# Optimization experiments

Measured on AMD Instinct MI355X. Metric: run time of the kernel, lower is better.

## Reference

```python
import jax, jax.numpy as jnp
import numpy as np

N_NODES = 100000
N_EDGES = 800000
NODE_DIM = 64
EDGE_DIM = 64
GEO_DIM = 8
GEO_OUT = 32
COND_DIM = 512
N_GRAPHS = 64
JOIN_DIM = EDGE_DIM + GEO_OUT  # 96


def setup_inputs() -> dict:
    key = jax.random.key(0)
    ks = jax.random.split(key, 10)
    return {
        "node_feats": jax.random.normal(ks[0], (N_NODES, NODE_DIM), jnp.float32),
        "edge_index": jax.random.randint(ks[1], (2, N_EDGES), 0, N_NODES, jnp.int64),
        "e_geo": jax.random.normal(ks[2], (N_EDGES, GEO_DIM), jnp.float32),
        "cond": jax.random.normal(ks[3], (N_GRAPHS, COND_DIM), jnp.float32),
        "edge_batch_ids": jax.random.randint(ks[4], (N_EDGES,), 0, N_GRAPHS, jnp.int64),
        "Wn": jax.random.normal(ks[5], (NODE_DIM, EDGE_DIM), jnp.float32) / np.sqrt(NODE_DIM),
        "bn": jnp.zeros((EDGE_DIM,), jnp.float32),
        "Wg": jax.random.normal(ks[6], (GEO_DIM, GEO_OUT), jnp.float32) / np.sqrt(GEO_DIM),
        "bg": jnp.zeros((GEO_OUT,), jnp.float32),
        "Wc": jax.random.normal(ks[7], (COND_DIM, 2 * EDGE_DIM), jnp.float32) / np.sqrt(COND_DIM),
        "bc": jnp.zeros((2 * EDGE_DIM,), jnp.float32),
        "Wx": jax.random.normal(ks[8], (JOIN_DIM, EDGE_DIM), jnp.float32) / np.sqrt(JOIN_DIM),
    }


def reference(node_feats, edge_index, e_geo, cond, edge_batch_ids,
              Wn, bn, Wg, bg, Wc, bc, Wx):
    # n_proj: project node features  [N, node_dim] -> [N, edge_dim]
    n_proj = node_feats @ Wn + bn
    # combine_node_attr 'mul': gather to edge endpoints and multiply  [E, edge_dim]
    src = n_proj[edge_index[0]]
    dst = n_proj[edge_index[1]]
    n_join = src * dst
    # e_geo_linear: [E, geo_dim] -> [E, geo_out]
    eg = e_geo @ Wg + bg
    # join features [E, edge_dim + geo_out]
    join = jnp.concatenate([n_join, eg], axis=-1)
    # FilmFusion: cond_proj -> gamma/beta per graph, gather to edges
    gb = cond @ Wc + bc                      # [B, 2*edge_dim]
    gamma, beta = jnp.split(gb, 2, axis=-1)
    gamma = gamma + 1.0
    gamma_e = gamma[edge_batch_ids]          # [E, edge_dim]
    beta_e = beta[edge_batch_ids]
    # x_linear (bias=False), FiLM modulation, relu
    x = join @ Wx
    return jax.nn.relu(x * gamma_e + beta_e)
```

## Files before the change

### kernel.cpp

```cpp
#include <hip/hip_runtime.h>

#define N_NODES   100000
#define N_EDGES   800000
#define NODE_DIM  64
#define EDGE_DIM  64
#define GEO_DIM   8
#define GEO_OUT   32
#define COND_DIM  512
#define N_GRAPHS  64

typedef short  bf8   __attribute__((ext_vector_type(8)));
typedef float  f32x4 __attribute__((ext_vector_type(4)));
typedef unsigned short u16x8 __attribute__((ext_vector_type(8)));

__device__ __forceinline__ float b2f(unsigned short u) {
    return __uint_as_float(((unsigned)u) << 16);
}
__device__ __forceinline__ short f2b(float f) {
    unsigned u = __float_as_uint(f);
    u = (u + 0x7FFFu + ((u >> 16) & 1u)) >> 16;
    return (short)u;
}
__device__ __forceinline__ float rdlane(float v, int l) {
    return __int_as_float(__builtin_amdgcn_readlane(__float_as_int(v), l));
}

__global__ __launch_bounds__(128) void prep_kernel(
        const float* __restrict__ cond, const float* __restrict__ Wc,
        const float* __restrict__ bc,   const float* __restrict__ Wg,
        const float* __restrict__ bg,   const float* __restrict__ Wx,
        float* __restrict__ gamma, float* __restrict__ beta2,
        unsigned short* __restrict__ Bmat) {
    int t = threadIdx.x;
    int g = blockIdx.x;
    if (g < N_GRAPHS) {
        __shared__ float condl[COND_DIM];
        __shared__ float gbl[128];
        for (int i = t; i < COND_DIM; i += 128) condl[i] = cond[g * COND_DIM + i];
        __syncthreads();
        float acc = bc[t];
        #pragma unroll 8
        for (int k = 0; k < COND_DIM; ++k) acc += condl[k] * Wc[k * 128 + t];
        gbl[t] = acc;
        __syncthreads();
        if (t < 64) {
            float gam = gbl[t] + 1.0f;
            float bet = gbl[64 + t];
            float cv = 0.0f;
            #pragma unroll
            for (int i = 0; i < GEO_OUT; ++i) cv += bg[i] * Wx[(64 + i) * 64 + t];
            gamma[g * 64 + t] = gam;
            beta2[g * 64 + t] = bet + cv * gam;
        }
    } else {
        for (int idx = t; idx < 64 * 64; idx += 128)
            Bmat[idx] = (unsigned short)f2b(Wx[idx]);
        for (int idx = t; idx < 8 * 64; idx += 128) {
            int r = idx >> 6, n = idx & 63;
            float s = 0.f;
            #pragma unroll
            for (int i = 0; i < GEO_OUT; ++i) s += Wg[r * GEO_OUT + i] * Wx[(64 + i) * 64 + n];
            Bmat[(64 + r) * 64 + n] = (unsigned short)f2b(s);
        }
        for (int idx = t; idx < 24 * 64; idx += 128)
            Bmat[72 * 64 + idx] = 0;
    }
}

__global__ __launch_bounds__(256) void nproj_kernel(
        const float* __restrict__ nf, const float* __restrict__ Wn,
        const float* __restrict__ bn, unsigned short* __restrict__ nprojb) {
    int lane = threadIdx.x & 63;
    int wid    = (blockIdx.x * blockDim.x + threadIdx.x) >> 6;
    int nwaves = (gridDim.x * blockDim.x) >> 6;
    float wcol[64];
    #pragma unroll
    for (int k = 0; k < 64; ++k) wcol[k] = Wn[k * 64 + lane];
    float bnl = bn[lane];
    for (int node = wid; node < N_NODES; node += nwaves) {
        float v = nf[(size_t)node * 64 + lane];
        float a0 = 0.f, a1 = 0.f, a2 = 0.f, a3 = bnl;
        #pragma unroll
        for (int k = 0; k < 64; k += 4) {
            a0 = fmaf(rdlane(v, k    ), wcol[k    ], a0);
            a1 = fmaf(rdlane(v, k + 1), wcol[k + 1], a1);
            a2 = fmaf(rdlane(v, k + 2), wcol[k + 2], a2);
            a3 = fmaf(rdlane(v, k + 3), wcol[k + 3], a3);
        }
        nprojb[(size_t)node * 64 + lane] = (unsigned short)f2b((a0 + a1) + (a2 + a3));
    }
}

__global__ __launch_bounds__(256) void edge_kernel(
        const unsigned short* __restrict__ nprojb,
        const int*   __restrict__ eidx,
        const float* __restrict__ egeo,
        const int*   __restrict__ ebatch,
        const unsigned short* __restrict__ Bmat,
        const float* __restrict__ gamma,
        const float* __restrict__ beta2,
        float* __restrict__ out) {
    int lane = threadIdx.x & 63;
    int q  = lane >> 4;
    int mm = lane & 15;
    int wid    = (blockIdx.x * blockDim.x + threadIdx.x) >> 6;
    int nwaves = (gridDim.x * blockDim.x) >> 6;

    bf8 bfrag[3][4];
    #pragma unroll
    for (int c = 0; c < 3; ++c)
        #pragma unroll
        for (int t = 0; t < 4; ++t)
            #pragma unroll
            for (int j = 0; j < 8; ++j)
                bfrag[c][t][j] = (short)Bmat[(c * 32 + q * 8 + j) * 64 + t * 16 + mm];

    const int NTILES = N_EDGES / 16;
    for (int tile = wid; tile < NTILES; tile += nwaves) {
        int e0 = tile * 16;
        int e  = e0 + mm;
        int s = __builtin_nontemporal_load(eidx + e);
        int d = __builtin_nontemporal_load(eidx + N_EDGES + e);
        const u16x8* ps = (const u16x8*)(nprojb + (size_t)s * 64 + q * 8);
        const u16x8* pd = (const u16x8*)(nprojb + (size_t)d * 64 + q * 8);
        u16x8 s0 = ps[0], s1 = ps[4];
        u16x8 d0 = pd[0], d1 = pd[4];
        bf8 a0, a1, a2;
        #pragma unroll
        for (int j = 0; j < 8; ++j) {
            a0[j] = f2b(b2f(s0[j]) * b2f(d0[j]));
            a1[j] = f2b(b2f(s1[j]) * b2f(d1[j]));
            a2[j] = 0;
        }
        if (q == 0) {
            f32x4 g0 = __builtin_nontemporal_load((const f32x4*)(egeo + (size_t)e * 8));
            f32x4 g1 = __builtin_nontemporal_load((const f32x4*)(egeo + (size_t)e * 8 + 4));
            #pragma unroll
            for (int j = 0; j < 4; ++j) { a2[j] = f2b(g0[j]); a2[4 + j] = f2b(g1[j]); }
        }

        f32x4 acc[4];
        #pragma unroll
        for (int t = 0; t < 4; ++t) {
            f32x4 c = {0.f, 0.f, 0.f, 0.f};
            c = __builtin_amdgcn_mfma_f32_16x16x32_bf16(a0, bfrag[0][t], c, 0, 0, 0);
            c = __builtin_amdgcn_mfma_f32_16x16x32_bf16(a1, bfrag[1][t], c, 0, 0, 0);
            c = __builtin_amdgcn_mfma_f32_16x16x32_bf16(a2, bfrag[2][t], c, 0, 0, 0);
            acc[t] = c;
        }

        #pragma unroll
        for (int i = 0; i < 4; ++i) {
            int row = q * 4 + i;
            int er  = e0 + row;
            int b   = __builtin_nontemporal_load(ebatch + er);
            const float* gp = gamma + b * 64;
            const float* bp = beta2 + b * 64;
            size_t ob = (size_t)er * 64;
            #pragma unroll
            for (int t = 0; t < 4; ++t) {
                int col = t * 16 + mm;
                float v = fmaf(acc[t][i], gp[col], bp[col]);
                __builtin_nontemporal_store(v > 0.f ? v : 0.f, out + ob + col);
            }
        }
    }
}

extern "C" void kernel_launch(void* const* d_in, const int* in_sizes, int n_in,
                              void* d_out, int out_size, void* d_ws, size_t ws_size,
                              hipStream_t stream) {
    const float* node_feats = (const float*)d_in[0];
    const int*   edge_index = (const int*)  d_in[1];
    const float* e_geo      = (const float*)d_in[2];
    const float* cond       = (const float*)d_in[3];
    const int*   ebatch     = (const int*)  d_in[4];
    const float* Wn         = (const float*)d_in[5];
    const float* bn         = (const float*)d_in[6];
    const float* Wg         = (const float*)d_in[7];
    const float* bg         = (const float*)d_in[8];
    const float* Wc         = (const float*)d_in[9];
    const float* bc         = (const float*)d_in[10];
    const float* Wx         = (const float*)d_in[11];
    float* out = (float*)d_out;

    char* ws = (char*)d_ws;
    float*          gamma  = (float*)(ws);
    float*          beta2  = (float*)(ws + 16384);
    unsigned short* Bmat   = (unsigned short*)(ws + 32768);
    unsigned short* nprojb = (unsigned short*)(ws + 49152);

    hipLaunchKernelGGL(prep_kernel, dim3(65), dim3(128), 0, stream,
                       cond, Wc, bc, Wg, bg, Wx, gamma, beta2, Bmat);
    hipLaunchKernelGGL(nproj_kernel, dim3(3125), dim3(256), 0, stream,
                       node_feats, Wn, bn, nprojb);
    hipLaunchKernelGGL(edge_kernel, dim3(6250), dim3(256), 0, stream,
                       nprojb, edge_index, e_geo, ebatch, Bmat, gamma, beta2, out);
}
```

Baseline: 387.2 us.

## Stage MFMA output through LDS for coalesced 16-byte stores and prepack B fragments

The edge kernel now writes each 16x64 MFMA accumulator tile into a per-wave LDS buffer and reads it back row-major, so each lane issues 16-byte vectorized nontemporal stores and vector gamma/beta loads. Before, each lane wrote scattered 4-byte elements. Batch IDs are prefetched before the gathers. The prep kernel also prepacks the B matrix into fragment order so each lane loads its fragments with one vector load. The product-to-bf16 conversions use paired bf16x2 conversions. The cost is 16 KB of LDS per block, which may limit occupancy, plus a wave-local LDS round trip ordered only by an lgkmcnt wait.

Result: faster. 373.0 us (-3.7%).

```diff
diff --git a/kernel.cpp b/kernel.cpp
--- a/kernel.cpp
+++ b/kernel.cpp
@@ -1,4 +1,5 @@
 #include <hip/hip_runtime.h>
+#include <hip/hip_bf16.h>
 
 #define N_NODES   100000
 #define N_EDGES   800000
@@ -21,6 +22,12 @@
     u = (u + 0x7FFFu + ((u >> 16) & 1u)) >> 16;
     return (short)u;
 }
+__device__ __forceinline__ unsigned f2b2(float lo, float hi) {
+    __hip_bfloat162 h = __float22bfloat162_rn(make_float2(lo, hi));
+    union { __hip_bfloat162 h; unsigned u; } cv;
+    cv.h = h;
+    return cv.u;
+}
 __device__ __forceinline__ float rdlane(float v, int l) {
     return __int_as_float(__builtin_amdgcn_readlane(__float_as_int(v), l));
 }
@@ -30,7 +37,7 @@
         const float* __restrict__ bc,   const float* __restrict__ Wg,
         const float* __restrict__ bg,   const float* __restrict__ Wx,
         float* __restrict__ gamma, float* __restrict__ beta2,
-        unsigned short* __restrict__ Bmat) {
+        unsigned short* __restrict__ Bfrag) {
     int t = threadIdx.x;
     int g = blockIdx.x;
     if (g < N_GRAPHS) {
@@ -53,17 +60,27 @@
             beta2[g * 64 + t] = bet + cv * gam;
         }
     } else {
-        for (int idx = t; idx < 64 * 64; idx += 128)
-            Bmat[idx] = (unsigned short)f2b(Wx[idx]);
-        for (int idx = t; idx < 8 * 64; idx += 128) {
-            int r = idx >> 6, n = idx & 63;
-            float s = 0.f;
-            #pragma unroll
-            for (int i = 0; i < GEO_OUT; ++i) s += Wg[r * GEO_OUT + i] * Wx[(64 + i) * 64 + n];
-            Bmat[(64 + r) * 64 + n] = (unsigned short)f2b(s);
-        }
-        for (int idx = t; idx < 24 * 64; idx += 128)
-            Bmat[72 * 64 + idx] = 0;
+        for (int idx = t; idx < 6144; idx += 128) {
+            int j    = idx & 7;
+            int lane = (idx >> 3) & 63;
+            int ct   = idx >> 9;
+            int c    = ct >> 2, tt = ct & 3;
+            int k = c * 32 + ((lane >> 4) & 3) * 8 + j;
+            int n = tt * 16 + (lane & 15);
+            float val;
+            if (k < 64) {
+                val = Wx[k * 64 + n];
+            } else if (k < 72) {
+                float s = 0.f;
+                #pragma unroll
+                for (int i = 0; i < GEO_OUT; ++i)
+                    s += Wg[(k - 64) * GEO_OUT + i] * Wx[(64 + i) * 64 + n];
+                val = s;
+            } else {
+                val = 0.f;
+            }
+            Bfrag[idx] = (unsigned short)f2b(val);
+        }
     }
 }
 
@@ -96,24 +113,26 @@
         const int*   __restrict__ eidx,
         const float* __restrict__ egeo,
         const int*   __restrict__ ebatch,
-        const unsigned short* __restrict__ Bmat,
+        const unsigned short* __restrict__ Bfrag,
         const float* __restrict__ gamma,
         const float* __restrict__ beta2,
         float* __restrict__ out) {
     int lane = threadIdx.x & 63;
     int q  = lane >> 4;
     int mm = lane & 15;
+    int wv = threadIdx.x >> 6;
     int wid    = (blockIdx.x * blockDim.x + threadIdx.x) >> 6;
     int nwaves = (gridDim.x * blockDim.x) >> 6;
+
+    __shared__ float ldsT[4][16 * 64];
+    float* tileb = ldsT[wv];
 
     bf8 bfrag[3][4];
     #pragma unroll
     for (int c = 0; c < 3; ++c)
         #pragma unroll
         for (int t = 0; t < 4; ++t)
-            #pragma unroll
-            for (int j = 0; j < 8; ++j)
-                bfrag[c][t][j] = (short)Bmat[(c * 32 + q * 8 + j) * 64 + t * 16 + mm];
+            bfrag[c][t] = *(const bf8*)(Bfrag + (size_t)((c * 4 + t) * 64 + lane) * 8);
 
     const int NTILES = N_EDGES / 16;
     for (int tile = wid; tile < NTILES; tile += nwaves) {
@@ -121,48 +140,63 @@
         int e  = e0 + mm;
         int s = __builtin_nontemporal_load(eidx + e);
         int d = __builtin_nontemporal_load(eidx + N_EDGES + e);
+        int bq[4];
+        #pragma unroll
+        for (int c = 0; c < 4; ++c)
+            bq[c] = __builtin_nontemporal_load(ebatch + e0 + c * 4 + q);
+
         const u16x8* ps = (const u16x8*)(nprojb + (size_t)s * 64 + q * 8);
         const u16x8* pd = (const u16x8*)(nprojb + (size_t)d * 64 + q * 8);
         u16x8 s0 = ps[0], s1 = ps[4];
         u16x8 d0 = pd[0], d1 = pd[4];
-        bf8 a0, a1, a2;
-        #pragma unroll
-        for (int j = 0; j < 8; ++j) {
-            a0[j] = f2b(b2f(s0[j]) * b2f(d0[j]));
-            a1[j] = f2b(b2f(s1[j]) * b2f(d1[j]));
-            a2[j] = 0;
+
+        union { bf8 v; unsigned u[4]; } A0, A1, A2;
+        #pragma unroll
+        for (int j = 0; j < 8; j += 2) {
+            A0.u[j >> 1] = f2b2(b2f(s0[j]) * b2f(d0[j]), b2f(s0[j + 1]) * b2f(d0[j + 1]));
+            A1.u[j >> 1] = f2b2(b2f(s1[j]) * b2f(d1[j]), b2f(s1[j + 1]) * b2f(d1[j + 1]));
+            A2.u[j >> 1] = 0u;
         }
         if (q == 0) {
             f32x4 g0 = __builtin_nontemporal_load((const f32x4*)(egeo + (size_t)e * 8));
             f32x4 g1 = __builtin_nontemporal_load((const f32x4*)(egeo + (size_t)e * 8 + 4));
-            #pragma unroll
-            for (int j = 0; j < 4; ++j) { a2[j] = f2b(g0[j]); a2[4 + j] = f2b(g1[j]); }
+            A2.u[0] = f2b2(g0[0], g0[1]);
+            A2.u[1] = f2b2(g0[2], g0[3]);
+            A2.u[2] = f2b2(g1[0], g1[1]);
+            A2.u[3] = f2b2(g1[2], g1[3]);
         }
 
         f32x4 acc[4];
         #pragma unroll
         for (int t = 0; t < 4; ++t) {
             f32x4 c = {0.f, 0.f, 0.f, 0.f};
-            c = __builtin_amdgcn_mfma_f32_16x16x32_bf16(a0, bfrag[0][t], c, 0, 0, 0);
-            c = __builtin_amdgcn_mfma_f32_16x16x32_bf16(a1, bfrag[1][t], c, 0, 0, 0);
-            c = __builtin_amdgcn_mfma_f32_16x16x32_bf16(a2, bfrag[2][t], c, 0, 0, 0);
+            c = __builtin_amdgcn_mfma_f32_16x16x32_bf16(A0.v, bfrag[0][t], c, 0, 0, 0);
+            c = __builtin_amdgcn_mfma_f32_16x16x32_bf16(A1.v, bfrag[1][t], c, 0, 0, 0);
+            c = __builtin_amdgcn_mfma_f32_16x16x32_bf16(A2.v, bfrag[2][t], c, 0, 0, 0);
             acc[t] = c;
         }
 
         #pragma unroll
-        for (int i = 0; i < 4; ++i) {
-            int row = q * 4 + i;
-            int er  = e0 + row;
-            int b   = __builtin_nontemporal_load(ebatch + er);
-            const float* gp = gamma + b * 64;
-            const float* bp = beta2 + b * 64;
-            size_t ob = (size_t)er * 64;
+        for (int t = 0; t < 4; ++t)
             #pragma unroll
-            for (int t = 0; t < 4; ++t) {
-                int col = t * 16 + mm;
-                float v = fmaf(acc[t][i], gp[col], bp[col]);
-                __builtin_nontemporal_store(v > 0.f ? v : 0.f, out + ob + col);
+            for (int i = 0; i < 4; ++i)
+                tileb[(q * 4 + i) * 64 + t * 16 + mm] = acc[t][i];
+        asm volatile("s_waitcnt lgkmcnt(0)" ::: "memory");
+
+        #pragma unroll
+        for (int c = 0; c < 4; ++c) {
+            int row = c * 4 + q;
+            int b   = bq[c];
+            f32x4 v  = *(const f32x4*)&tileb[row * 64 + mm * 4];
+            f32x4 gm = *(const f32x4*)(gamma + b * 64 + mm * 4);
+            f32x4 bt = *(const f32x4*)(beta2 + b * 64 + mm * 4);
+            f32x4 r;
+            #pragma unroll
+            for (int i = 0; i < 4; ++i) {
+                float x = fmaf(v[i], gm[i], bt[i]);
+                r[i] = x > 0.f ? x : 0.f;
             }
+            __builtin_nontemporal_store(r, (f32x4*)(out + (size_t)e0 * 64 + c * 256 + lane * 4));
         }
     }
 }
@@ -187,13 +221,13 @@
     char* ws = (char*)d_ws;
     float*          gamma  = (float*)(ws);
     float*          beta2  = (float*)(ws + 16384);
-    unsigned short* Bmat   = (unsigned short*)(ws + 32768);
+    unsigned short* Bfrag  = (unsigned short*)(ws + 32768);
     unsigned short* nprojb = (unsigned short*)(ws + 49152);
 
     hipLaunchKernelGGL(prep_kernel, dim3(65), dim3(128), 0, stream,
-                       cond, Wc, bc, Wg, bg, Wx, gamma, beta2, Bmat);
+                       cond, Wc, bc, Wg, bg, Wx, gamma, beta2, Bfrag);
     hipLaunchKernelGGL(nproj_kernel, dim3(3125), dim3(256), 0, stream,
                        node_feats, Wn, bn, nprojb);
     hipLaunchKernelGGL(edge_kernel, dim3(6250), dim3(256), 0, stream,
-                       nprojb, edge_index, e_geo, ebatch, Bmat, gamma, beta2, out);
-}
+                       nprojb, edge_index, e_geo, ebatch, Bfrag, gamma, beta2, out);
+}
```
